# Kernel optimization log

Measured on AMD Instinct MI355X. Metric: run time of the kernel, lower is better.

The kernel has to match this reference:

```python
import jax, jax.numpy as jnp
import numpy as np

P_DROP = 0.1
NTYPES = 8
DROP_KEY = jax.random.key(42)


def _dropout(h, i):
    # deterministic training-mode dropout, mask fixed by layer index
    keep = jax.random.bernoulli(jax.random.fold_in(DROP_KEY, i), 1.0 - P_DROP, h.shape)
    return jnp.where(keep, h / (1.0 - P_DROP), 0.0).astype(h.dtype)


def _func_conv(h, src, dst, types, convW, convb, act):
    # gather src features along edges, mean-aggregate onto dst nodes,
    # then apply a per-gate-type linear transform.
    n_out = types.shape[0]
    msg = h[src]                                                  # [E, d]
    agg = jax.ops.segment_sum(msg, dst, num_segments=n_out)       # [n_out, d]
    deg = jax.ops.segment_sum(jnp.ones((src.shape[0],), h.dtype), dst,
                              num_segments=n_out)
    agg = agg / jnp.maximum(deg, 1.0)[:, None]
    out = jnp.zeros((n_out, convW.shape[2]), h.dtype)
    for t in range(convW.shape[0]):                                # ntypes is small & fixed
        mask = (types == t).astype(h.dtype)[:, None]
        out = out + (agg * mask) @ convW[t]
    out = out + convb[types]
    return jax.nn.relu(out) if act else out


def setup_inputs() -> dict:
    key = jax.random.key(0)
    ks = jax.random.split(key, 16)
    N0, N1, N2, N3 = 400_000, 200_000, 100_000, 50_000
    E0, E1, E2 = 1_600_000, 800_000, 400_000
    d, dout = 128, 64
    inp = {
        "features": jax.random.normal(ks[0], (N0, d), jnp.float32),
        "src0": jax.random.randint(ks[1], (E0,), 0, N0),
        "dst0": jax.random.randint(ks[2], (E0,), 0, N1),
        "types1": jax.random.randint(ks[3], (N1,), 0, NTYPES),
        "src1": jax.random.randint(ks[4], (E1,), 0, N1),
        "dst1": jax.random.randint(ks[5], (E1,), 0, N2),
        "types2": jax.random.randint(ks[6], (N2,), 0, NTYPES),
        "src2": jax.random.randint(ks[7], (E2,), 0, N2),
        "dst2": jax.random.randint(ks[8], (E2,), 0, N3),
        "types3": jax.random.randint(ks[9], (N3,), 0, NTYPES),
        # learned params
        "convW": jax.random.normal(ks[10], (NTYPES, d, d), jnp.float32) / np.sqrt(d),
        "convb": jnp.zeros((NTYPES, d), jnp.float32),
        "fcW": jax.random.normal(ks[11], (d, dout), jnp.float32) / np.sqrt(d),
        "fcb": jnp.zeros((dout,), jnp.float32),
    }
    return inp


def reference(features, src0, dst0, types1, src1, dst1, types2,
              src2, dst2, types3, convW, convb, fcW, fcb):
    blocks = [(src0, dst0, types1), (src1, dst1, types2), (src2, dst2, types3)]
    depth = len(blocks)
    h = features
    for i, (s, dst, t) in enumerate(blocks):
        if i != 0:
            h = _dropout(h, i)
        h = _func_conv(h, s, dst, t, convW, convb, act=(i != depth - 1))
    h = h @ fcW + fcb   # hidden_dim != out_dim -> fc_out applied
    return h            # squeeze(1) is a no-op for out_dim > 1
```

## Files before the change

kernel.cpp:

```cpp
#include <hip/hip_runtime.h>
#include <cstdint>
#include <cstddef>

__host__ __device__ inline void tf2x32(uint32_t k0, uint32_t k1,
                                       uint32_t x0, uint32_t x1,
                                       uint32_t* o0, uint32_t* o1)
{
    uint32_t ks2 = k0 ^ k1 ^ 0x1BD11BDAu;
    x0 += k0; x1 += k1;
#define TF_R(r) do { x0 += x1; x1 = (x1 << (r)) | (x1 >> (32 - (r))); x1 ^= x0; } while (0)
    TF_R(13); TF_R(15); TF_R(26); TF_R(6);
    x0 += k1;  x1 += ks2 + 1u;
    TF_R(17); TF_R(29); TF_R(16); TF_R(24);
    x0 += ks2; x1 += k0 + 2u;
    TF_R(13); TF_R(15); TF_R(26); TF_R(6);
    x0 += k0;  x1 += k1 + 3u;
    TF_R(17); TF_R(29); TF_R(16); TF_R(24);
    x0 += k1;  x1 += ks2 + 4u;
    TF_R(13); TF_R(15); TF_R(26); TF_R(6);
    x0 += ks2; x1 += k0 + 5u;
#undef TF_R
    *o0 = x0; *o1 = x1;
}

__device__ inline float drop_scale(uint32_t fk0, uint32_t fk1, uint32_t idx)
{
    uint32_t o0, o1;
    tf2x32(fk0, fk1, 0u, idx, &o0, &o1);
    uint32_t bits = o0 ^ o1;
    float u = __uint_as_float((bits >> 9) | 0x3f800000u) - 1.0f;
    return (u < 0.9f) ? (1.0f / 0.9f) : 0.0f;
}

__device__ inline ushort bf16_rn(float f)
{
    uint32_t u = __float_as_uint(f);
    u += 0x7fffu + ((u >> 16) & 1u);
    return (ushort)(u >> 16);
}
__device__ inline float bf16_f(ushort h) { return __uint_as_float(((uint32_t)h) << 16); }
__device__ inline uint32_t pack2bf(float a, float b)
{
    return (uint32_t)bf16_rn(a) | ((uint32_t)bf16_rn(b) << 16);
}
__device__ inline float bflo(uint32_t u) { return __uint_as_float(u << 16); }
__device__ inline float bfhi(uint32_t u) { return __uint_as_float(u & 0xffff0000u); }

typedef __attribute__((ext_vector_type(8))) short bf16x8;
typedef __attribute__((ext_vector_type(4))) float f32x4;

__global__ __launch_bounds__(256) void fcvt_kernel(
    const float4* __restrict__ in, uint2* __restrict__ out, long long n4)
{
    long long stride = (long long)gridDim.x * 256;
    for (long long i = blockIdx.x * 256LL + threadIdx.x; i < n4; i += stride) {
        float4 v = in[i];
        out[i] = make_uint2(pack2bf(v.x, v.y), pack2bf(v.z, v.w));
    }
}

#define EPB 4096

__global__ __launch_bounds__(256) void bcount3_kernel(
    const int* __restrict__ d0, const int* __restrict__ d1, const int* __restrict__ d2,
    int E0, int E1, int E2, int nb0, int nb1, int nb2,
    int nblk0, int nblk1, int nblk2, uint32_t* __restrict__ tot)
{
    int L = blockIdx.y;
    const int* dst = L == 0 ? d0 : (L == 1 ? d1 : d2);
    int E  = L == 0 ? E0 : (L == 1 ? E1 : E2);
    int NB = L == 0 ? nb0 : (L == 1 ? nb1 : nb2);
    int nblk = L == 0 ? nblk0 : (L == 1 ? nblk1 : nblk2);
    int gO = L == 0 ? 0 : (L == 1 ? nb0 : nb0 + nb1);
    if ((int)blockIdx.x >= nblk) return;

    __shared__ uint32_t lh[256];
    int tid = threadIdx.x;
    lh[tid] = 0;
    __syncthreads();
    int base = blockIdx.x * EPB;
    for (int i = tid; i < EPB; i += 256) {
        int e = base + i;
        if (e < E) atomicAdd(&lh[((uint32_t)dst[e]) >> 10], 1u);
    }
    __syncthreads();
    if (tid < NB && lh[tid]) atomicAdd(&tot[gO + tid], lh[tid]);
}

__global__ __launch_bounds__(512) void bscan_small_kernel(
    const uint32_t* __restrict__ tot, uint32_t* __restrict__ bo,
    uint32_t* __restrict__ bcur, uint32_t* __restrict__ rowptr3,
    int nb0, int nb1, int nb2, int N1, int N2, int N3, int r1, int r2)
{
    __shared__ uint32_t bol[348];
    int t = threadIdx.x;
    int TB = nb0 + nb1 + nb2;
    if (t < 3) {
        int nb = t == 0 ? nb0 : (t == 1 ? nb1 : nb2);
        int g0 = t == 0 ? 0 : (t == 1 ? nb0 : nb0 + nb1);
        int gi0 = g0 + t;
        uint32_t run = 0;
        for (int i = 0; i < nb; ++i) { bol[gi0 + i] = run; run += tot[g0 + i]; }
        bol[gi0 + nb] = run;
        int rp = t == 0 ? 0 : (t == 1 ? r1 : r2);
        int N = t == 0 ? N1 : (t == 1 ? N2 : N3);
        rowptr3[rp + N] = run;
    }
    __syncthreads();
    for (int i = t; i < TB + 3; i += 512) bo[i] = bol[i];
    if (t < TB) {
        int layer = t < nb0 ? 0 : (t < nb0 + nb1 ? 1 : 2);
        bcur[t] = bol[t + layer];
    }
}

__global__ __launch_bounds__(256) void bscatter3_kernel(
    const int* __restrict__ s0, const int* __restrict__ d0,
    const int* __restrict__ s1, const int* __restrict__ d1,
    const int* __restrict__ s2, const int* __restrict__ d2,
    int E0, int E1, int E2, int nb0, int nb1, int nb2,
    int nblk0, int nblk1, int nblk2,
    uint32_t* __restrict__ bcur, uint32_t* __restrict__ pairs)
{
    int L = blockIdx.y;
    const int* src = L == 0 ? s0 : (L == 1 ? s1 : s2);
    const int* dst = L == 0 ? d0 : (L == 1 ? d1 : d2);
    int E  = L == 0 ? E0 : (L == 1 ? E1 : E2);
    int NB = L == 0 ? nb0 : (L == 1 ? nb1 : nb2);
    int nblk = L == 0 ? nblk0 : (L == 1 ? nblk1 : nblk2);
    int gO = L == 0 ? 0 : (L == 1 ? nb0 : nb0 + nb1);
    uint32_t* pr = pairs + (L == 0 ? 0 : (L == 1 ? E0 : E0 + E1));
    if ((int)blockIdx.x >= nblk) return;

    __shared__ uint32_t lh[256], lbase[256], rank[256];
    int tid = threadIdx.x;
    lh[tid] = 0; rank[tid] = 0;
    __syncthreads();
    int base = blockIdx.x * EPB;
    for (int i = tid; i < EPB; i += 256) {
        int e = base + i;
        if (e < E) atomicAdd(&lh[((uint32_t)dst[e]) >> 10], 1u);
    }
    __syncthreads();
    if (tid < NB && lh[tid]) lbase[tid] = atomicAdd(&bcur[gO + tid], lh[tid]);
    __syncthreads();
    for (int i = tid; i < EPB; i += 256) {
        int e = base + i;
        if (e < E) {
            uint32_t d = (uint32_t)dst[e];
            uint32_t bk = d >> 10;
            uint32_t r = atomicAdd(&rank[bk], 1u);
            pr[lbase[bk] + r] = ((d & 1023u) << 22) | (uint32_t)src[e];
        }
    }
}

__global__ __launch_bounds__(256) void bfill_kernel(
    const uint32_t* __restrict__ bo, const uint32_t* __restrict__ pairs,
    int* __restrict__ elist3, uint32_t* __restrict__ rowptr3,
    int nb0, int nb1, int nb2, int N1, int N2, int N3,
    int E0, int E1, int r1, int r2)
{
    __shared__ uint32_t hist[1024];
    __shared__ uint32_t cur[1024];
    __shared__ uint32_t psum[256];
    int g = blockIdx.x, tid = threadIdx.x;
    int layer, lb, N, Eoff, rp;
    if (g < nb0) { layer = 0; lb = g; N = N1; Eoff = 0; rp = 0; }
    else if (g < nb0 + nb1) { layer = 1; lb = g - nb0; N = N2; Eoff = E0; rp = r1; }
    else { layer = 2; lb = g - nb0 - nb1; N = N3; Eoff = E0 + E1; rp = r2; }
    uint32_t off = bo[g + layer], end = bo[g + layer + 1];
    int nodeBase = lb << 10;
    int nodesIn = N - nodeBase; if (nodesIn > 1024) nodesIn = 1024;

    #pragma unroll
    for (int i = 0; i < 4; ++i) hist[tid * 4 + i] = 0;
    __syncthreads();
    for (uint32_t e = off + tid; e < end; e += 256)
        atomicAdd(&hist[pairs[Eoff + e] >> 22], 1u);
    __syncthreads();

    uint32_t x[4]; uint32_t s = 0;
    #pragma unroll
    for (int i = 0; i < 4; ++i) { x[i] = hist[tid * 4 + i]; s += x[i]; }
    psum[tid] = s; __syncthreads();
    uint32_t inc = s;
    #pragma unroll
    for (int o = 1; o < 256; o <<= 1) {
        uint32_t y = (tid >= o) ? psum[tid - o] : 0u;
        __syncthreads();
        inc += y; psum[tid] = inc;
        __syncthreads();
    }
    uint32_t run = off + inc - s;
    #pragma unroll
    for (int i = 0; i < 4; ++i) { cur[tid * 4 + i] = run; run += x[i]; }
    __syncthreads();

    for (int i = tid; i < nodesIn; i += 256)
        rowptr3[rp + nodeBase + i] = cur[i];
    __syncthreads();

    for (uint32_t e = off + tid; e < end; e += 256) {
        uint32_t pk = pairs[Eoff + e];
        uint32_t pos = atomicAdd(&cur[pk >> 22], 1u);
        elist3[Eoff + pos] = (int)(pk & 0x3FFFFFu);
    }
}

__global__ __launch_bounds__(256) void count3_kernel(
    const int* __restrict__ t0, const int* __restrict__ t1, const int* __restrict__ t2,
    int n0, int n1, int n2, uint32_t* __restrict__ tcnt)
{
    __shared__ uint32_t lh[24];
    int tid = threadIdx.x;
    if (tid < 24) lh[tid] = 0;
    __syncthreads();
    int i = blockIdx.x * 256 + tid;
    if (i < n0) atomicAdd(&lh[t0[i]], 1u);
    else if (i < n0 + n1) atomicAdd(&lh[8 + t1[i - n0]], 1u);
    else if (i < n0 + n1 + n2) atomicAdd(&lh[16 + t2[i - n0 - n1]], 1u);
    __syncthreads();
    if (tid < 24 && lh[tid]) atomicAdd(&tcnt[tid], lh[tid]);
}

__global__ __launch_bounds__(256) void scan_types3_kernel(
    const uint32_t* __restrict__ tcnt, int* __restrict__ boff,
    uint32_t* __restrict__ tcur, int* __restrict__ order3, int no1p, int no2p)
{
    __shared__ int pB[27];
    __shared__ int cnts[24];
    int tid = threadIdx.x;
    if (tid == 0) {
        for (int L = 0; L < 3; ++L) {
            int a = 0;
            for (int t = 0; t < 8; ++t) {
                pB[L * 9 + t] = a;
                int c = (int)tcnt[L * 8 + t];
                cnts[L * 8 + t] = c;
                tcur[L * 8 + t] = (uint32_t)a;
                a += (c + 127) & ~127;
            }
            pB[L * 9 + 8] = a;
        }
    }
    __syncthreads();
    if (tid < 27) boff[tid] = pB[tid];
    if (tid < 24) {
        int L = tid >> 3, t = tid & 7;
        int noff = L == 0 ? 0 : (L == 1 ? no1p : no2p);
        int s = pB[L * 9 + t] + cnts[tid];
        int e2 = pB[L * 9 + t + 1];
        for (int k = s; k < e2; ++k) order3[noff + k] = -1;
    }
}

__global__ __launch_bounds__(256) void order3_kernel(
    const int* __restrict__ t0, const int* __restrict__ t1, const int* __restrict__ t2,
    int n0, int n1, int n2, uint32_t* __restrict__ tcur,
    int* __restrict__ order3, int no1p, int no2p)
{
    __shared__ uint32_t lh[24], lbase[24];
    int tid = threadIdx.x;
    if (tid < 24) lh[tid] = 0;
    __syncthreads();
    int i = blockIdx.x * 256 + tid;
    int slot = -1, idx = 0; uint32_t r = 0;
    if (i < n0) { idx = i; slot = t0[idx]; }
    else if (i < n0 + n1) { idx = i - n0; slot = 8 + t1[idx]; }
    else if (i < n0 + n1 + n2) { idx = i - n0 - n1; slot = 16 + t2[idx]; }
    if (slot >= 0) r = atomicAdd(&lh[slot], 1u);
    __syncthreads();
    if (tid < 24 && lh[tid]) lbase[tid] = atomicAdd(&tcur[tid], lh[tid]);
    __syncthreads();
    if (slot >= 0) {
        int noff = slot < 8 ? 0 : (slot < 16 ? no1p : no2p);
        order3[noff + lbase[slot] + r] = idx;
    }
}

__global__ __launch_bounds__(256) void aggregate_kernel(
    const uint32_t* __restrict__ hbf, const uint32_t* __restrict__ rowptr,
    const int* __restrict__ elist, uint32_t* __restrict__ agghi,
    uint32_t* __restrict__ agglo, int nout)
{
    int wid = threadIdx.x >> 6, lane = threadIdx.x & 63;
    int n0 = blockIdx.x * 8 + wid * 2;
    if (n0 >= nout) return;
    int n1 = n0 + 1;
    bool v1 = (n1 < nout);
    uint32_t b0 = rowptr[n0], e0 = rowptr[n0 + 1];
    uint32_t b1 = v1 ? rowptr[n1] : 0u, e1 = v1 ? rowptr[n1 + 1] : 0u;
    const uint32_t* base = hbf + lane;
    float a0x = 0.f, a0y = 0.f, a1x = 0.f, a1y = 0.f;
    uint32_t i0 = b0, i1 = b1;

    while (i0 + 8 <= e0 && i1 + 8 <= e1) {
        uint32_t u[8], w[8];
        #pragma unroll
        for (int k = 0; k < 8; ++k) u[k] = base[(size_t)elist[i0 + k] * 64];
        #pragma unroll
        for (int k = 0; k < 8; ++k) w[k] = base[(size_t)elist[i1 + k] * 64];
        #pragma unroll
        for (int k = 0; k < 8; ++k) { a0x += bflo(u[k]); a0y += bfhi(u[k]); }
        #pragma unroll
        for (int k = 0; k < 8; ++k) { a1x += bflo(w[k]); a1y += bfhi(w[k]); }
        i0 += 8; i1 += 8;
    }
    while (i0 + 4 <= e0 && i1 + 4 <= e1) {
        uint32_t u[4], w[4];
        #pragma unroll
        for (int k = 0; k < 4; ++k) u[k] = base[(size_t)elist[i0 + k] * 64];
        #pragma unroll
        for (int k = 0; k < 4; ++k) w[k] = base[(size_t)elist[i1 + k] * 64];
        #pragma unroll
        for (int k = 0; k < 4; ++k) { a0x += bflo(u[k]); a0y += bfhi(u[k]); }
        #pragma unroll
        for (int k = 0; k < 4; ++k) { a1x += bflo(w[k]); a1y += bfhi(w[k]); }
        i0 += 4; i1 += 4;
    }
    while (i0 + 4 <= e0) {
        uint32_t u[4];
        #pragma unroll
        for (int k = 0; k < 4; ++k) u[k] = base[(size_t)elist[i0 + k] * 64];
        #pragma unroll
        for (int k = 0; k < 4; ++k) { a0x += bflo(u[k]); a0y += bfhi(u[k]); }
        i0 += 4;
    }
    while (i1 + 4 <= e1) {
        uint32_t w[4];
        #pragma unroll
        for (int k = 0; k < 4; ++k) w[k] = base[(size_t)elist[i1 + k] * 64];
        #pragma unroll
        for (int k = 0; k < 4; ++k) { a1x += bflo(w[k]); a1y += bfhi(w[k]); }
        i1 += 4;
    }
    for (; i0 < e0; ++i0) {
        uint32_t u = base[(size_t)elist[i0] * 64];
        a0x += bflo(u); a0y += bfhi(u);
    }
    for (; i1 < e1; ++i1) {
        uint32_t w = base[(size_t)elist[i1] * 64];
        a1x += bflo(w); a1y += bfhi(w);
    }

    float sc0 = 1.0f / fmaxf((float)(e0 - b0), 1.0f);
    a0x *= sc0; a0y *= sc0;
    ushort hx = bf16_rn(a0x); ushort lx = bf16_rn(a0x - bf16_f(hx));
    ushort hy = bf16_rn(a0y); ushort ly = bf16_rn(a0y - bf16_f(hy));
    agghi[(size_t)n0 * 64 + lane] = (uint32_t)hx | ((uint32_t)hy << 16);
    agglo[(size_t)n0 * 64 + lane] = (uint32_t)lx | ((uint32_t)ly << 16);
    if (v1) {
        float sc1 = 1.0f / fmaxf((float)(e1 - b1), 1.0f);
        a1x *= sc1; a1y *= sc1;
        ushort hx1 = bf16_rn(a1x); ushort lx1 = bf16_rn(a1x - bf16_f(hx1));
        ushort hy1 = bf16_rn(a1y); ushort ly1 = bf16_rn(a1y - bf16_f(hy1));
        agghi[(size_t)n1 * 64 + lane] = (uint32_t)hx1 | ((uint32_t)hy1 << 16);
        agglo[(size_t)n1 * 64 + lane] = (uint32_t)lx1 | ((uint32_t)ly1 << 16);
    }
}

__global__ __launch_bounds__(256) void prep_wt_kernel(
    const float* __restrict__ src8, ushort* __restrict__ dsthi,
    ushort* __restrict__ dstlo, int C)
{
    int t = blockIdx.x;
    const float* S = src8 + (size_t)t * 128 * C;
    ushort* DH = dsthi + (size_t)t * C * 128;
    ushort* DL = dstlo + (size_t)t * C * 128;
    for (int idx = threadIdx.x; idx < 128 * C; idx += 256) {
        int k = idx / C, c = idx % C;
        float v = S[(size_t)k * C + c];
        ushort hi = bf16_rn(v);
        ushort lo = bf16_rn(v - bf16_f(hi));
        int pos = c * 128 + ((((k >> 3) ^ (c & 15)) << 3) | (k & 7));
        DH[pos] = hi; DL[pos] = lo;
    }
}

template<int DOUT, bool RELU, bool DROP, bool OUTBF>
__global__ __launch_bounds__(512) void mfma_gemm_kernel(
    const uint32_t* __restrict__ agghi, const uint32_t* __restrict__ agglo,
    const int* __restrict__ order, const int* __restrict__ off,
    const ushort* __restrict__ WThi, const ushort* __restrict__ WTlo,
    const float* __restrict__ bias8, void* __restrict__ houtv,
    uint32_t fk0, uint32_t fk1)
{
    __shared__ ushort WH[DOUT * 128];
    __shared__ ushort WL[DOUT * 128];
    __shared__ int ND[128];

    int b0 = blockIdx.x * 128;
    if (b0 >= off[8]) return;
    int t = 0;
    #pragma unroll
    for (int u = 1; u < 8; ++u) if (b0 >= off[u]) ++t;
    int tid = threadIdx.x;

    if (tid < 128) ND[tid] = order[b0 + tid];

    {
        const float4* sh = (const float4*)(WThi + (size_t)t * DOUT * 128);
        const float4* sl = (const float4*)(WTlo + (size_t)t * DOUT * 128);
        float4* dh = (float4*)WH; float4* dl = (float4*)WL;
        #pragma unroll
        for (int it = 0; it < DOUT * 16 / 512; ++it) {
            int c = it * 512 + tid;
            dh[c] = sh[c]; dl[c] = sl[c];
        }
    }
    __syncthreads();

    int wid = tid >> 6, lane = tid & 63;
    int r15 = lane & 15, q = lane >> 4;
    int arow = wid * 16 + r15;
    int nd_a = ND[arow];

    const bf16x8* gh = (const bf16x8*)agghi;
    const bf16x8* gl = (const bf16x8*)agglo;
    bf16x8 zero8 = (bf16x8){0, 0, 0, 0, 0, 0, 0, 0};
    bf16x8 ahv[4], alv[4];
    {
        size_t rowb = (size_t)(nd_a < 0 ? 0 : nd_a) * 16;
        #pragma unroll
        for (int ks = 0; ks < 4; ++ks) {
            size_t ix = rowb + (q + ks * 4);
            ahv[ks] = (nd_a >= 0) ? gh[ix] : zero8;
            alv[ks] = (nd_a >= 0) ? gl[ix] : zero8;
        }
    }

    constexpr int NF = DOUT / 16;
    f32x4 acc[NF];
    #pragma unroll
    for (int i = 0; i < NF; ++i) acc[i] = (f32x4){0.f, 0.f, 0.f, 0.f};

    const bf16x8* WHp = (const bf16x8*)WH;
    const bf16x8* WLp = (const bf16x8*)WL;

    #pragma unroll
    for (int ks = 0; ks < 4; ++ks) {
        int sch = (q + ks * 4) ^ r15;
        bf16x8 ah = ahv[ks];
        bf16x8 al = alv[ks];
        #pragma unroll
        for (int nf = 0; nf < NF; ++nf) {
            int col = nf * 16 + r15;
            bf16x8 bh = WHp[col * 16 + sch];
            bf16x8 bl = WLp[col * 16 + sch];
            acc[nf] = __builtin_amdgcn_mfma_f32_16x16x32_bf16(ah, bh, acc[nf], 0, 0, 0);
            acc[nf] = __builtin_amdgcn_mfma_f32_16x16x32_bf16(ah, bl, acc[nf], 0, 0, 0);
            acc[nf] = __builtin_amdgcn_mfma_f32_16x16x32_bf16(al, bh, acc[nf], 0, 0, 0);
        }
    }

    int ndr[4];
    #pragma unroll
    for (int r = 0; r < 4; ++r) ndr[r] = ND[wid * 16 + q * 4 + r];
    const float* bptr = bias8 + (size_t)t * DOUT;

    #pragma unroll
    for (int nf = 0; nf < NF; ++nf) {
        int col = nf * 16 + r15;
        float bv = bptr[col];
        float vr[4];
        #pragma unroll
        for (int r = 0; r < 4; ++r) {
            float v = acc[nf][r] + bv;
            if (RELU) v = fmaxf(v, 0.f);
            if (DROP) {
                int nd = ndr[r] < 0 ? 0 : ndr[r];
                v *= drop_scale(fk0, fk1, (uint32_t)nd * 128u + (uint32_t)col);
            }
            vr[r] = v;
        }
        if (OUTBF) {
            uint32_t* hb = (uint32_t*)houtv;
            #pragma unroll
            for (int r = 0; r < 4; ++r) {
                float w = __shfl_xor(vr[r], 1, 64);
                if ((lane & 1) == 0 && ndr[r] >= 0)
                    hb[(size_t)ndr[r] * (DOUT / 2) + (col >> 1)] = pack2bf(vr[r], w);
            }
        } else {
            float* ho = (float*)houtv;
            #pragma unroll
            for (int r = 0; r < 4; ++r)
                if (ndr[r] >= 0) ho[(size_t)ndr[r] * DOUT + col] = vr[r];
        }
    }
}

__global__ __launch_bounds__(256) void fuse_fc_kernel(
    const float* __restrict__ convW, const float* __restrict__ convb,
    const float* __restrict__ fcW, const float* __restrict__ fcb,
    float* __restrict__ Wf, float* __restrict__ bf)
{
    __shared__ float F[128 * 64];
    int t = blockIdx.x, tid = threadIdx.x;
    #pragma unroll
    for (int it = 0; it < 8; ++it) {
        int idx4 = (it * 256 + tid) * 4;
        *(float4*)&F[idx4] = *(const float4*)&fcW[idx4];
    }
    __syncthreads();

    int r = tid >> 1, cb = (tid & 1) * 32;
    const float* Wrow = convW + (size_t)t * 16384 + (size_t)r * 128;
    float acc[32];
    #pragma unroll
    for (int c = 0; c < 32; ++c) acc[c] = 0.f;
    for (int k = 0; k < 128; ++k) {
        float w = Wrow[k];
        #pragma unroll
        for (int c = 0; c < 32; ++c) acc[c] += w * F[k * 64 + cb + c];
    }
    float* outp = Wf + (size_t)t * 8192 + (size_t)r * 64 + cb;
    #pragma unroll
    for (int c = 0; c < 32; ++c) outp[c] = acc[c];

    if (tid < 64) {
        float a = fcb[tid];
        const float* bt = convb + (size_t)t * 128;
        for (int k = 0; k < 128; ++k) a += bt[k] * F[k * 64 + tid];
        bf[(size_t)t * 64 + tid] = a;
    }
}

extern "C" void kernel_launch(void* const* d_in, const int* in_sizes, int n_in,
                              void* d_out, int out_size, void* d_ws, size_t ws_size,
                              hipStream_t stream)
{
    const float* features = (const float*)d_in[0];
    const int*   src0 = (const int*)d_in[1];
    const int*   dst0 = (const int*)d_in[2];
    const int*   types1 = (const int*)d_in[3];
    const int*   src1 = (const int*)d_in[4];
    const int*   dst1 = (const int*)d_in[5];
    const int*   types2 = (const int*)d_in[6];
    const int*   src2 = (const int*)d_in[7];
    const int*   dst2 = (const int*)d_in[8];
    const int*   types3 = (const int*)d_in[9];
    const float* convW = (const float*)d_in[10];
    const float* convb = (const float*)d_in[11];
    const float* fcW   = (const float*)d_in[12];
    const float* fcb   = (const float*)d_in[13];

    int N0 = in_sizes[0] / 128;
    int E0 = in_sizes[1], N1 = in_sizes[3];
    int E1 = in_sizes[4], N2 = in_sizes[6];
    int E2 = in_sizes[7], N3 = in_sizes[9];
    int totalN = N1 + N2 + N3;
    int totalE = E0 + E1 + E2;
    int r1 = N1 + 1, r2 = N1 + 1 + N2 + 1;
    int no1p = N1 + 1024, no2p = no1p + N2 + 1024;
    int maxN = N1 > N2 ? N1 : N2; if (N3 > maxN) maxN = N3;

    int nb0 = (N1 + 1023) >> 10, nb1 = (N2 + 1023) >> 10, nb2 = (N3 + 1023) >> 10;
    int TB = nb0 + nb1 + nb2;
    int nblk0 = (E0 + EPB - 1) / EPB, nblk1 = (E1 + EPB - 1) / EPB, nblk2 = (E2 + EPB - 1) / EPB;
    int nblkMax = nblk0 > nblk1 ? nblk0 : nblk1; if (nblk2 > nblkMax) nblkMax = nblk2;

    char* ws = (char*)d_ws;
    size_t woff = 0;
    auto alloc = [&](size_t bytes) -> void* {
        void* p = ws + woff;
        woff = (woff + bytes + 255) & ~(size_t)255;
        return p;
    };
    uint32_t* fbf     = (uint32_t*)alloc((size_t)N0 * 64 * 4);
    uint32_t* hbf     = fbf;
    uint32_t* aggHi   = (uint32_t*)alloc((size_t)maxN * 64 * 4);
    uint32_t* pairs   = aggHi;
    uint32_t* aggLo   = (uint32_t*)alloc((size_t)maxN * 64 * 4);
    uint32_t* rowptr3 = (uint32_t*)alloc((size_t)(totalN + 3) * 4);
    int*      elist3  = (int*)alloc((size_t)totalE * 4);
    int*      order3  = (int*)alloc((size_t)(totalN + 3 * 1024) * 4);
    uint32_t* tot     = (uint32_t*)alloc((size_t)(TB + 8) * 4);
    uint32_t* bcur    = (uint32_t*)alloc((size_t)(TB + 8) * 4);
    uint32_t* bo      = (uint32_t*)alloc((size_t)(TB + 3) * 4);
    uint32_t* tcnt    = (uint32_t*)alloc(24 * 4);
    int*      boff    = (int*)alloc(27 * 4);
    uint32_t* tcur    = (uint32_t*)alloc(24 * 4);
    float*    Wf      = (float*)alloc((size_t)8 * 128 * 64 * 4);
    float*    bfb     = (float*)alloc((size_t)8 * 64 * 4);
    ushort*   WThi    = (ushort*)alloc((size_t)8 * 128 * 128 * 2);
    ushort*   WTlo    = (ushort*)alloc((size_t)8 * 128 * 128 * 2);
    ushort*   WfThi   = (ushort*)alloc((size_t)8 * 64 * 128 * 2);
    ushort*   WfTlo   = (ushort*)alloc((size_t)8 * 64 * 128 * 2);
    (void)ws_size; (void)n_in; (void)out_size;

    fcvt_kernel<<<4096, 256, 0, stream>>>(
        (const float4*)features, (uint2*)fbf, (long long)N0 * 32);
    prep_wt_kernel<<<8, 256, 0, stream>>>(convW, WThi, WTlo, 128);
    fuse_fc_kernel<<<8, 256, 0, stream>>>(convW, convb, fcW, fcb, Wf, bfb);
    prep_wt_kernel<<<8, 256, 0, stream>>>(Wf, WfThi, WfTlo, 64);

    hipMemsetAsync(tot, 0, (size_t)TB * 4, stream);
    bcount3_kernel<<<dim3(nblkMax, 3), 256, 0, stream>>>(
        dst0, dst1, dst2, E0, E1, E2, nb0, nb1, nb2,
        nblk0, nblk1, nblk2, tot);
    bscan_small_kernel<<<1, 512, 0, stream>>>(tot, bo, bcur, rowptr3,
        nb0, nb1, nb2, N1, N2, N3, r1, r2);
    bscatter3_kernel<<<dim3(nblkMax, 3), 256, 0, stream>>>(
        src0, dst0, src1, dst1, src2, dst2, E0, E1, E2, nb0, nb1, nb2,
        nblk0, nblk1, nblk2, bcur, pairs);
    bfill_kernel<<<TB, 256, 0, stream>>>(bo, pairs, elist3, rowptr3,
        nb0, nb1, nb2, N1, N2, N3, E0, E1, r1, r2);

    hipMemsetAsync(tcnt, 0, 24 * 4, stream);
    int nblkT = (totalN + 255) / 256;
    count3_kernel<<<nblkT, 256, 0, stream>>>(types1, types2, types3, N1, N2, N3, tcnt);
    scan_types3_kernel<<<1, 256, 0, stream>>>(tcnt, boff, tcur, order3, no1p, no2p);
    order3_kernel<<<nblkT, 256, 0, stream>>>(
        types1, types2, types3, N1, N2, N3, tcur, order3, no1p, no2p);

    uint32_t fk1a, fk1b, fk2a, fk2b;
    tf2x32(0u, 42u, 0u, 1u, &fk1a, &fk1b);
    tf2x32(0u, 42u, 0u, 2u, &fk2a, &fk2b);

    aggregate_kernel<<<(N1 + 7) / 8, 256, 0, stream>>>(
        fbf, rowptr3, elist3, aggHi, aggLo, N1);
    mfma_gemm_kernel<128, true, true, true><<<(N1 + 127) / 128 + 8, 512, 0, stream>>>(
        aggHi, aggLo, order3, boff, WThi, WTlo, convb, hbf, fk1a, fk1b);

    aggregate_kernel<<<(N2 + 7) / 8, 256, 0, stream>>>(
        hbf, rowptr3 + r1, elist3 + E0, aggHi, aggLo, N2);
    mfma_gemm_kernel<128, true, true, true><<<(N2 + 127) / 128 + 8, 512, 0, stream>>>(
        aggHi, aggLo, order3 + no1p, boff + 9, WThi, WTlo, convb, hbf, fk2a, fk2b);

    aggregate_kernel<<<(N3 + 7) / 8, 256, 0, stream>>>(
        hbf, rowptr3 + r2, elist3 + E0 + E1, aggHi, aggLo, N3);
    mfma_gemm_kernel<64, false, false, false><<<(N3 + 127) / 128 + 8, 512, 0, stream>>>(
        aggHi, aggLo, order3 + no2p, boff + 18, WfThi, WfTlo, bfb, d_out, 0u, 0u);
}
```

Measured before the change: 566.2 us.

## Merge preprocessing kernels and software-pipeline edge index loads in aggregation

Fuses the three weight-prep kernels into one prep_all kernel. It also merges the edge bucket histogram/scatter with the node-type count/order passes into shared 4-row grids with a single combined scan, which cuts kernel launches and a memset. The aggregate kernel now prefetches the next batch of edge indices while gathering the current rows, to hide the dependent index-load latency. The cost is higher register pressure and larger combined kernels that have divergent roles per blockIdx.y.

```diff
diff --git a/kernel.cpp b/kernel.cpp
--- a/kernel.cpp
+++ b/kernel.cpp
@@ -59,40 +59,123 @@
     }
 }
 
+__global__ __launch_bounds__(256) void prep_all_kernel(
+    const float* __restrict__ convW, const float* __restrict__ convb,
+    const float* __restrict__ fcW, const float* __restrict__ fcb,
+    ushort* __restrict__ WThi, ushort* __restrict__ WTlo,
+    ushort* __restrict__ WfThi, ushort* __restrict__ WfTlo,
+    float* __restrict__ bfb)
+{
+    __shared__ float F[128 * 64];
+    int t = blockIdx.x, tid = threadIdx.x;
+    #pragma unroll
+    for (int it = 0; it < 8; ++it) {
+        int idx4 = (it * 256 + tid) * 4;
+        *(float4*)&F[idx4] = *(const float4*)&fcW[idx4];
+    }
+    __syncthreads();
+
+    {
+        const float* S = convW + (size_t)t * 16384;
+        ushort* DH = WThi + (size_t)t * 16384;
+        ushort* DL = WTlo + (size_t)t * 16384;
+        for (int idx = tid; idx < 16384; idx += 256) {
+            int k = idx >> 7, c = idx & 127;
+            float v = S[idx];
+            ushort hi = bf16_rn(v);
+            ushort lo = bf16_rn(v - bf16_f(hi));
+            int pos = c * 128 + ((((k >> 3) ^ (c & 15)) << 3) | (k & 7));
+            DH[pos] = hi; DL[pos] = lo;
+        }
+    }
+
+    {
+        int r = tid >> 1, cb = (tid & 1) * 32;
+        const float* Wrow = convW + (size_t)t * 16384 + (size_t)r * 128;
+        float acc[32];
+        #pragma unroll
+        for (int c = 0; c < 32; ++c) acc[c] = 0.f;
+        for (int k = 0; k < 128; ++k) {
+            float w = Wrow[k];
+            #pragma unroll
+            for (int c = 0; c < 32; ++c) acc[c] += w * F[k * 64 + cb + c];
+        }
+        ushort* FH = WfThi + (size_t)t * 8192;
+        ushort* FL = WfTlo + (size_t)t * 8192;
+        int swzr = (r & 7);
+        #pragma unroll
+        for (int c = 0; c < 32; ++c) {
+            int col = cb + c;
+            float v = acc[c];
+            ushort hi = bf16_rn(v);
+            ushort lo = bf16_rn(v - bf16_f(hi));
+            int pos = col * 128 + ((((r >> 3) ^ (col & 15)) << 3) | swzr);
+            FH[pos] = hi; FL[pos] = lo;
+        }
+    }
+
+    if (tid < 64) {
+        float a = fcb[tid];
+        const float* bt = convb + (size_t)t * 128;
+        for (int k = 0; k < 128; ++k) a += bt[k] * F[k * 64 + tid];
+        bfb[(size_t)t * 64 + tid] = a;
+    }
+}
+
 #define EPB 4096
 
-__global__ __launch_bounds__(256) void bcount3_kernel(
+__global__ __launch_bounds__(256) void hist_all_kernel(
     const int* __restrict__ d0, const int* __restrict__ d1, const int* __restrict__ d2,
-    int E0, int E1, int E2, int nb0, int nb1, int nb2,
-    int nblk0, int nblk1, int nblk2, uint32_t* __restrict__ tot)
+    const int* __restrict__ t1, const int* __restrict__ t2, const int* __restrict__ t3,
+    int E0, int E1, int E2, int N1, int N2, int N3,
+    int nb0, int nb1, int nb2, int nblk0, int nblk1, int nblk2,
+    uint32_t* __restrict__ tot, uint32_t* __restrict__ tcnt)
 {
     int L = blockIdx.y;
-    const int* dst = L == 0 ? d0 : (L == 1 ? d1 : d2);
-    int E  = L == 0 ? E0 : (L == 1 ? E1 : E2);
-    int NB = L == 0 ? nb0 : (L == 1 ? nb1 : nb2);
-    int nblk = L == 0 ? nblk0 : (L == 1 ? nblk1 : nblk2);
-    int gO = L == 0 ? 0 : (L == 1 ? nb0 : nb0 + nb1);
-    if ((int)blockIdx.x >= nblk) return;
-
-    __shared__ uint32_t lh[256];
     int tid = threadIdx.x;
-    lh[tid] = 0;
-    __syncthreads();
-    int base = blockIdx.x * EPB;
-    for (int i = tid; i < EPB; i += 256) {
-        int e = base + i;
-        if (e < E) atomicAdd(&lh[((uint32_t)dst[e]) >> 10], 1u);
-    }
-    __syncthreads();
-    if (tid < NB && lh[tid]) atomicAdd(&tot[gO + tid], lh[tid]);
-}
-
-__global__ __launch_bounds__(512) void bscan_small_kernel(
+    if (L < 3) {
+        const int* dst = L == 0 ? d0 : (L == 1 ? d1 : d2);
+        int E  = L == 0 ? E0 : (L == 1 ? E1 : E2);
+        int NB = L == 0 ? nb0 : (L == 1 ? nb1 : nb2);
+        int nblk = L == 0 ? nblk0 : (L == 1 ? nblk1 : nblk2);
+        int gO = L == 0 ? 0 : (L == 1 ? nb0 : nb0 + nb1);
+        if ((int)blockIdx.x >= nblk) return;
+        __shared__ uint32_t lh[256];
+        lh[tid] = 0;
+        __syncthreads();
+        int base = blockIdx.x * EPB;
+        for (int i = tid; i < EPB; i += 256) {
+            int e = base + i;
+            if (e < E) atomicAdd(&lh[((uint32_t)dst[e]) >> 10], 1u);
+        }
+        __syncthreads();
+        if (tid < NB && lh[tid]) atomicAdd(&tot[gO + tid], lh[tid]);
+    } else {
+        int totalN = N1 + N2 + N3;
+        if ((int)blockIdx.x * 256 >= totalN) return;
+        __shared__ uint32_t lh[24];
+        if (tid < 24) lh[tid] = 0;
+        __syncthreads();
+        int i = blockIdx.x * 256 + tid;
+        if (i < N1) atomicAdd(&lh[t1[i]], 1u);
+        else if (i < N1 + N2) atomicAdd(&lh[8 + t2[i - N1]], 1u);
+        else if (i < totalN) atomicAdd(&lh[16 + t3[i - N1 - N2]], 1u);
+        __syncthreads();
+        if (tid < 24 && lh[tid]) atomicAdd(&tcnt[tid], lh[tid]);
+    }
+}
+
+__global__ __launch_bounds__(512) void scan_all_kernel(
     const uint32_t* __restrict__ tot, uint32_t* __restrict__ bo,
     uint32_t* __restrict__ bcur, uint32_t* __restrict__ rowptr3,
-    int nb0, int nb1, int nb2, int N1, int N2, int N3, int r1, int r2)
+    const uint32_t* __restrict__ tcnt, int* __restrict__ boff,
+    uint32_t* __restrict__ tcur, int* __restrict__ order3,
+    int nb0, int nb1, int nb2, int N1, int N2, int N3,
+    int r1, int r2, int no1p, int no2p)
 {
     __shared__ uint32_t bol[348];
+    __shared__ int pB[27];
+    __shared__ int cnts[24];
     int t = threadIdx.x;
     int TB = nb0 + nb1 + nb2;
     if (t < 3) {
@@ -106,51 +189,95 @@
         int N = t == 0 ? N1 : (t == 1 ? N2 : N3);
         rowptr3[rp + N] = run;
     }
+    if (t == 3) {
+        for (int L = 0; L < 3; ++L) {
+            int a = 0;
+            for (int ty = 0; ty < 8; ++ty) {
+                pB[L * 9 + ty] = a;
+                int c = (int)tcnt[L * 8 + ty];
+                cnts[L * 8 + ty] = c;
+                tcur[L * 8 + ty] = (uint32_t)a;
+                a += (c + 127) & ~127;
+            }
+            pB[L * 9 + 8] = a;
+        }
+    }
     __syncthreads();
     for (int i = t; i < TB + 3; i += 512) bo[i] = bol[i];
     if (t < TB) {
         int layer = t < nb0 ? 0 : (t < nb0 + nb1 ? 1 : 2);
         bcur[t] = bol[t + layer];
     }
-}
-
-__global__ __launch_bounds__(256) void bscatter3_kernel(
+    if (t < 27) boff[t] = pB[t];
+    if (t < 24) {
+        int L = t >> 3, ty = t & 7;
+        int noff = L == 0 ? 0 : (L == 1 ? no1p : no2p);
+        int s = pB[L * 9 + ty] + cnts[t];
+        int e2 = pB[L * 9 + ty + 1];
+        for (int k = s; k < e2; ++k) order3[noff + k] = -1;
+    }
+}
+
+__global__ __launch_bounds__(256) void scatter_all_kernel(
     const int* __restrict__ s0, const int* __restrict__ d0,
     const int* __restrict__ s1, const int* __restrict__ d1,
     const int* __restrict__ s2, const int* __restrict__ d2,
-    int E0, int E1, int E2, int nb0, int nb1, int nb2,
-    int nblk0, int nblk1, int nblk2,
-    uint32_t* __restrict__ bcur, uint32_t* __restrict__ pairs)
+    const int* __restrict__ t1, const int* __restrict__ t2, const int* __restrict__ t3,
+    int E0, int E1, int E2, int N1, int N2, int N3,
+    int nb0, int nb1, int nb2, int nblk0, int nblk1, int nblk2,
+    uint32_t* __restrict__ bcur, uint32_t* __restrict__ pairs,
+    uint32_t* __restrict__ tcur, int* __restrict__ order3, int no1p, int no2p)
 {
     int L = blockIdx.y;
-    const int* src = L == 0 ? s0 : (L == 1 ? s1 : s2);
-    const int* dst = L == 0 ? d0 : (L == 1 ? d1 : d2);
-    int E  = L == 0 ? E0 : (L == 1 ? E1 : E2);
-    int NB = L == 0 ? nb0 : (L == 1 ? nb1 : nb2);
-    int nblk = L == 0 ? nblk0 : (L == 1 ? nblk1 : nblk2);
-    int gO = L == 0 ? 0 : (L == 1 ? nb0 : nb0 + nb1);
-    uint32_t* pr = pairs + (L == 0 ? 0 : (L == 1 ? E0 : E0 + E1));
-    if ((int)blockIdx.x >= nblk) return;
-
-    __shared__ uint32_t lh[256], lbase[256], rank[256];
     int tid = threadIdx.x;
-    lh[tid] = 0; rank[tid] = 0;
-    __syncthreads();
-    int base = blockIdx.x * EPB;
-    for (int i = tid; i < EPB; i += 256) {
-        int e = base + i;
-        if (e < E) atomicAdd(&lh[((uint32_t)dst[e]) >> 10], 1u);
-    }
-    __syncthreads();
-    if (tid < NB && lh[tid]) lbase[tid] = atomicAdd(&bcur[gO + tid], lh[tid]);
-    __syncthreads();
-    for (int i = tid; i < EPB; i += 256) {
-        int e = base + i;
-        if (e < E) {
-            uint32_t d = (uint32_t)dst[e];
-            uint32_t bk = d >> 10;
-            uint32_t r = atomicAdd(&rank[bk], 1u);
-            pr[lbase[bk] + r] = ((d & 1023u) << 22) | (uint32_t)src[e];
+    if (L < 3) {
+        const int* src = L == 0 ? s0 : (L == 1 ? s1 : s2);
+        const int* dst = L == 0 ? d0 : (L == 1 ? d1 : d2);
+        int E  = L == 0 ? E0 : (L == 1 ? E1 : E2);
+        int NB = L == 0 ? nb0 : (L == 1 ? nb1 : nb2);
+        int nblk = L == 0 ? nblk0 : (L == 1 ? nblk1 : nblk2);
+        int gO = L == 0 ? 0 : (L == 1 ? nb0 : nb0 + nb1);
+        uint32_t* pr = pairs + (L == 0 ? 0 : (L == 1 ? E0 : E0 + E1));
+        if ((int)blockIdx.x >= nblk) return;
+
+        __shared__ uint32_t lh[256], lbase[256], rank[256];
+        lh[tid] = 0; rank[tid] = 0;
+        __syncthreads();
+        int base = blockIdx.x * EPB;
+        for (int i = tid; i < EPB; i += 256) {
+            int e = base + i;
+            if (e < E) atomicAdd(&lh[((uint32_t)dst[e]) >> 10], 1u);
+        }
+        __syncthreads();
+        if (tid < NB && lh[tid]) lbase[tid] = atomicAdd(&bcur[gO + tid], lh[tid]);
+        __syncthreads();
+        for (int i = tid; i < EPB; i += 256) {
+            int e = base + i;
+            if (e < E) {
+                uint32_t d = (uint32_t)dst[e];
+                uint32_t bk = d >> 10;
+                uint32_t r = atomicAdd(&rank[bk], 1u);
+                pr[lbase[bk] + r] = ((d & 1023u) << 22) | (uint32_t)src[e];
+            }
+        }
+    } else {
+        int totalN = N1 + N2 + N3;
+        if ((int)blockIdx.x * 256 >= totalN) return;
+        __shared__ uint32_t lh[24], lbase[24];
+        if (tid < 24) lh[tid] = 0;
+        __syncthreads();
+        int i = blockIdx.x * 256 + tid;
+        int slot = -1, idx = 0; uint32_t r = 0;
+        if (i < N1) { idx = i; slot = t1[idx]; }
+        else if (i < N1 + N2) { idx = i - N1; slot = 8 + t2[idx]; }
+        else if (i < totalN) { idx = i - N1 - N2; slot = 16 + t3[idx]; }
+        if (slot >= 0) r = atomicAdd(&lh[slot], 1u);
+        __syncthreads();
+        if (tid < 24 && lh[tid]) lbase[tid] = atomicAdd(&tcur[tid], lh[tid]);
+        __syncthreads();
+        if (slot >= 0) {
+            int noff = slot < 8 ? 0 : (slot < 16 ? no1p : no2p);
+            order3[noff + lbase[slot] + r] = idx;
         }
     }
 }
@@ -208,77 +335,6 @@
     }
 }
 
-__global__ __launch_bounds__(256) void count3_kernel(
-    const int* __restrict__ t0, const int* __restrict__ t1, const int* __restrict__ t2,
-    int n0, int n1, int n2, uint32_t* __restrict__ tcnt)
-{
-    __shared__ uint32_t lh[24];
-    int tid = threadIdx.x;
-    if (tid < 24) lh[tid] = 0;
-    __syncthreads();
-    int i = blockIdx.x * 256 + tid;
-    if (i < n0) atomicAdd(&lh[t0[i]], 1u);
-    else if (i < n0 + n1) atomicAdd(&lh[8 + t1[i - n0]], 1u);
-    else if (i < n0 + n1 + n2) atomicAdd(&lh[16 + t2[i - n0 - n1]], 1u);
-    __syncthreads();
-    if (tid < 24 && lh[tid]) atomicAdd(&tcnt[tid], lh[tid]);
-}
-
-__global__ __launch_bounds__(256) void scan_types3_kernel(
-    const uint32_t* __restrict__ tcnt, int* __restrict__ boff,
-    uint32_t* __restrict__ tcur, int* __restrict__ order3, int no1p, int no2p)
-{
-    __shared__ int pB[27];
-    __shared__ int cnts[24];
-    int tid = threadIdx.x;
-    if (tid == 0) {
-        for (int L = 0; L < 3; ++L) {
-            int a = 0;
-            for (int t = 0; t < 8; ++t) {
-                pB[L * 9 + t] = a;
-                int c = (int)tcnt[L * 8 + t];
-                cnts[L * 8 + t] = c;
-                tcur[L * 8 + t] = (uint32_t)a;
-                a += (c + 127) & ~127;
-            }
-            pB[L * 9 + 8] = a;
-        }
-    }
-    __syncthreads();
-    if (tid < 27) boff[tid] = pB[tid];
-    if (tid < 24) {
-        int L = tid >> 3, t = tid & 7;
-        int noff = L == 0 ? 0 : (L == 1 ? no1p : no2p);
-        int s = pB[L * 9 + t] + cnts[tid];
-        int e2 = pB[L * 9 + t + 1];
-        for (int k = s; k < e2; ++k) order3[noff + k] = -1;
-    }
-}
-
-__global__ __launch_bounds__(256) void order3_kernel(
-    const int* __restrict__ t0, const int* __restrict__ t1, const int* __restrict__ t2,
-    int n0, int n1, int n2, uint32_t* __restrict__ tcur,
-    int* __restrict__ order3, int no1p, int no2p)
-{
-    __shared__ uint32_t lh[24], lbase[24];
-    int tid = threadIdx.x;
-    if (tid < 24) lh[tid] = 0;
-    __syncthreads();
-    int i = blockIdx.x * 256 + tid;
-    int slot = -1, idx = 0; uint32_t r = 0;
-    if (i < n0) { idx = i; slot = t0[idx]; }
-    else if (i < n0 + n1) { idx = i - n0; slot = 8 + t1[idx]; }
-    else if (i < n0 + n1 + n2) { idx = i - n0 - n1; slot = 16 + t2[idx]; }
-    if (slot >= 0) r = atomicAdd(&lh[slot], 1u);
-    __syncthreads();
-    if (tid < 24 && lh[tid]) lbase[tid] = atomicAdd(&tcur[tid], lh[tid]);
-    __syncthreads();
-    if (slot >= 0) {
-        int noff = slot < 8 ? 0 : (slot < 16 ? no1p : no2p);
-        order3[noff + lbase[slot] + r] = idx;
-    }
-}
-
 __global__ __launch_bounds__(256) void aggregate_kernel(
     const uint32_t* __restrict__ hbf, const uint32_t* __restrict__ rowptr,
     const int* __restrict__ elist, uint32_t* __restrict__ agghi,
@@ -295,17 +351,28 @@
     float a0x = 0.f, a0y = 0.f, a1x = 0.f, a1y = 0.f;
     uint32_t i0 = b0, i1 = b1;
 
-    while (i0 + 8 <= e0 && i1 + 8 <= e1) {
-        uint32_t u[8], w[8];
-        #pragma unroll
-        for (int k = 0; k < 8; ++k) u[k] = base[(size_t)elist[i0 + k] * 64];
-        #pragma unroll
-        for (int k = 0; k < 8; ++k) w[k] = base[(size_t)elist[i1 + k] * 64];
-        #pragma unroll
-        for (int k = 0; k < 8; ++k) { a0x += bflo(u[k]); a0y += bfhi(u[k]); }
-        #pragma unroll
-        for (int k = 0; k < 8; ++k) { a1x += bflo(w[k]); a1y += bfhi(w[k]); }
-        i0 += 8; i1 += 8;
+    if (i0 + 8 <= e0 && i1 + 8 <= e1) {
+        int ia[8], ib[8];
+        #pragma unroll
+        for (int k = 0; k < 8; ++k) { ia[k] = elist[i0 + k]; ib[k] = elist[i1 + k]; }
+        for (;;) {
+            uint32_t u[8], w[8];
+            #pragma unroll
+            for (int k = 0; k < 8; ++k) u[k] = base[(size_t)ia[k] * 64];
+            #pragma unroll
+            for (int k = 0; k < 8; ++k) w[k] = base[(size_t)ib[k] * 64];
+            i0 += 8; i1 += 8;
+            bool more = (i0 + 8 <= e0 && i1 + 8 <= e1);
+            if (more) {
+                #pragma unroll
+                for (int k = 0; k < 8; ++k) { ia[k] = elist[i0 + k]; ib[k] = elist[i1 + k]; }
+            }
+            #pragma unroll
+            for (int k = 0; k < 8; ++k) { a0x += bflo(u[k]); a0y += bfhi(u[k]); }
+            #pragma unroll
+            for (int k = 0; k < 8; ++k) { a1x += bflo(w[k]); a1y += bfhi(w[k]); }
+            if (!more) break;
+        }
     }
     while (i0 + 4 <= e0 && i1 + 4 <= e1) {
         uint32_t u[4], w[4];
@@ -360,24 +427,6 @@
     }
 }
 
-__global__ __launch_bounds__(256) void prep_wt_kernel(
-    const float* __restrict__ src8, ushort* __restrict__ dsthi,
-    ushort* __restrict__ dstlo, int C)
-{
-    int t = blockIdx.x;
-    const float* S = src8 + (size_t)t * 128 * C;
-    ushort* DH = dsthi + (size_t)t * C * 128;
-    ushort* DL = dstlo + (size_t)t * C * 128;
-    for (int idx = threadIdx.x; idx < 128 * C; idx += 256) {
-        int k = idx / C, c = idx % C;
-        float v = S[(size_t)k * C + c];
-        ushort hi = bf16_rn(v);
-        ushort lo = bf16_rn(v - bf16_f(hi));
-        int pos = c * 128 + ((((k >> 3) ^ (c & 15)) << 3) | (k & 7));
-        DH[pos] = hi; DL[pos] = lo;
-    }
-}
-
 template<int DOUT, bool RELU, bool DROP, bool OUTBF>
 __global__ __launch_bounds__(512) void mfma_gemm_kernel(
     const uint32_t* __restrict__ agghi, const uint32_t* __restrict__ agglo,
@@ -488,42 +537,6 @@
             for (int r = 0; r < 4; ++r)
                 if (ndr[r] >= 0) ho[(size_t)ndr[r] * DOUT + col] = vr[r];
         }
-    }
-}
-
-__global__ __launch_bounds__(256) void fuse_fc_kernel(
-    const float* __restrict__ convW, const float* __restrict__ convb,
-    const float* __restrict__ fcW, const float* __restrict__ fcb,
-    float* __restrict__ Wf, float* __restrict__ bf)
-{
-    __shared__ float F[128 * 64];
-    int t = blockIdx.x, tid = threadIdx.x;
-    #pragma unroll
-    for (int it = 0; it < 8; ++it) {
-        int idx4 = (it * 256 + tid) * 4;
-        *(float4*)&F[idx4] = *(const float4*)&fcW[idx4];
-    }
-    __syncthreads();
-
-    int r = tid >> 1, cb = (tid & 1) * 32;
-    const float* Wrow = convW + (size_t)t * 16384 + (size_t)r * 128;
-    float acc[32];
-    #pragma unroll
-    for (int c = 0; c < 32; ++c) acc[c] = 0.f;
-    for (int k = 0; k < 128; ++k) {
-        float w = Wrow[k];
-        #pragma unroll
-        for (int c = 0; c < 32; ++c) acc[c] += w * F[k * 64 + cb + c];
-    }
-    float* outp = Wf + (size_t)t * 8192 + (size_t)r * 64 + cb;
-    #pragma unroll
-    for (int c = 0; c < 32; ++c) outp[c] = acc[c];
-
-    if (tid < 64) {
-        float a = fcb[tid];
-        const float* bt = convb + (size_t)t * 128;
-        for (int k = 0; k < 128; ++k) a += bt[k] * F[k * 64 + tid];
-        bf[(size_t)t * 64 + tid] = a;
     }
 }
 
@@ -560,6 +573,8 @@
     int TB = nb0 + nb1 + nb2;
     int nblk0 = (E0 + EPB - 1) / EPB, nblk1 = (E1 + EPB - 1) / EPB, nblk2 = (E2 + EPB - 1) / EPB;
     int nblkMax = nblk0 > nblk1 ? nblk0 : nblk1; if (nblk2 > nblkMax) nblkMax = nblk2;
+    int nblkT = (totalN + 255) / 256;
+    int gx = nblkMax > nblkT ? nblkMax : nblkT;
 
     char* ws = (char*)d_ws;
     size_t woff = 0;
@@ -576,13 +591,12 @@
     uint32_t* rowptr3 = (uint32_t*)alloc((size_t)(totalN + 3) * 4);
     int*      elist3  = (int*)alloc((size_t)totalE * 4);
     int*      order3  = (int*)alloc((size_t)(totalN + 3 * 1024) * 4);
-    uint32_t* tot     = (uint32_t*)alloc((size_t)(TB + 8) * 4);
+    uint32_t* tot     = (uint32_t*)alloc((size_t)(TB + 8 + 24) * 4);
+    uint32_t* tcnt    = tot + TB + 8;
     uint32_t* bcur    = (uint32_t*)alloc((size_t)(TB + 8) * 4);
     uint32_t* bo      = (uint32_t*)alloc((size_t)(TB + 3) * 4);
-    uint32_t* tcnt    = (uint32_t*)alloc(24 * 4);
     int*      boff    = (int*)alloc(27 * 4);
     uint32_t* tcur    = (uint32_t*)alloc(24 * 4);
-    float*    Wf      = (float*)alloc((size_t)8 * 128 * 64 * 4);
     float*    bfb     = (float*)alloc((size_t)8 * 64 * 4);
     ushort*   WThi    = (ushort*)alloc((size_t)8 * 128 * 128 * 2);
     ushort*   WTlo    = (ushort*)alloc((size_t)8 * 128 * 128 * 2);
@@ -592,28 +606,22 @@
 
     fcvt_kernel<<<4096, 256, 0, stream>>>(
         (const float4*)features, (uint2*)fbf, (long long)N0 * 32);
-    prep_wt_kernel<<<8, 256, 0, stream>>>(convW, WThi, WTlo, 128);
-    fuse_fc_kernel<<<8, 256, 0, stream>>>(convW, convb, fcW, fcb, Wf, bfb);
-    prep_wt_kernel<<<8, 256, 0, stream>>>(Wf, WfThi, WfTlo, 64);
-
-    hipMemsetAsync(tot, 0, (size_t)TB * 4, stream);
-    bcount3_kernel<<<dim3(nblkMax, 3), 256, 0, stream>>>(
-        dst0, dst1, dst2, E0, E1, E2, nb0, nb1, nb2,
-        nblk0, nblk1, nblk2, tot);
-    bscan_small_kernel<<<1, 512, 0, stream>>>(tot, bo, bcur, rowptr3,
-        nb0, nb1, nb2, N1, N2, N3, r1, r2);
-    bscatter3_kernel<<<dim3(nblkMax, 3), 256, 0, stream>>>(
-        src0, dst0, src1, dst1, src2, dst2, E0, E1, E2, nb0, nb1, nb2,
-        nblk0, nblk1, nblk2, bcur, pairs);
+    prep_all_kernel<<<8, 256, 0, stream>>>(
+        convW, convb, fcW, fcb, WThi, WTlo, WfThi, WfTlo, bfb);
+
+    hipMemsetAsync(tot, 0, (size_t)(TB + 8 + 24) * 4, stream);
+    hist_all_kernel<<<dim3(gx, 4), 256, 0, stream>>>(
+        dst0, dst1, dst2, types1, types2, types3,
+        E0, E1, E2, N1, N2, N3, nb0, nb1, nb2, nblk0, nblk1, nblk2, tot, tcnt);
+    scan_all_kernel<<<1, 512, 0, stream>>>(
+        tot, bo, bcur, rowptr3, tcnt, boff, tcur, order3,
+        nb0, nb1, nb2, N1, N2, N3, r1, r2, no1p, no2p);
+    scatter_all_kernel<<<dim3(gx, 4), 256, 0, stream>>>(
+        src0, dst0, src1, dst1, src2, dst2, types1, types2, types3,
+        E0, E1, E2, N1, N2, N3, nb0, nb1, nb2, nblk0, nblk1, nblk2,
+        bcur, pairs, tcur, order3, no1p, no2p);
     bfill_kernel<<<TB, 256, 0, stream>>>(bo, pairs, elist3, rowptr3,
         nb0, nb1, nb2, N1, N2, N3, E0, E1, r1, r2);
-
-    hipMemsetAsync(tcnt, 0, 24 * 4, stream);
-    int nblkT = (totalN + 255) / 256;
-    count3_kernel<<<nblkT, 256, 0, stream>>>(types1, types2, types3, N1, N2, N3, tcnt);
-    scan_types3_kernel<<<1, 256, 0, stream>>>(tcnt, boff, tcur, order3, no1p, no2p);
-    order3_kernel<<<nblkT, 256, 0, stream>>>(
-        types1, types2, types3, N1, N2, N3, tcur, order3, no1p, no2p);
 
     uint32_t fk1a, fk1b, fk2a, fk2b;
     tf2x32(0u, 42u, 0u, 1u, &fk1a, &fk1b);
```

After: 581.9 us. +2.8%, slower.
